# Kernel optimization log

Measured on AMD Instinct MI355X. Metric: run time of the kernel, lower is better.

Reference implementation:

```python
import jax, jax.numpy as jnp
import numpy as np

PROJ_EPS = 1e-5   # hyperbolic_projection keeps ||x|| <= 1 - PROJ_EPS
MIN_NORM = 1e-15  # numerical floor for norms/denominators
N, D, E, L = 100000, 128, 800000, 2


def _norm(x):
    return jnp.linalg.norm(x, axis=-1, keepdims=True)


def hyperbolic_projection(x):
    n = _norm(x)
    max_n = 1.0 - PROJ_EPS
    scale = jnp.where(n > max_n, max_n / jnp.maximum(n, MIN_NORM), 1.0)
    return x * scale


def exp_map_zero(v):
    n = jnp.maximum(_norm(v), MIN_NORM)
    return jnp.tanh(n) * v / n


def log_map_zero(y):
    n = jnp.maximum(_norm(y), MIN_NORM)
    nc = jnp.clip(n, MIN_NORM, 1.0 - PROJ_EPS)
    return jnp.arctanh(nc) * y / n


def mobius_addition(u, v):
    uu = jnp.sum(u * u, -1, keepdims=True)
    vv = jnp.sum(v * v, -1, keepdims=True)
    uv = jnp.sum(u * v, -1, keepdims=True)
    num = (1.0 + 2.0 * uv + vv) * u + (1.0 - uu) * v
    den = 1.0 + 2.0 * uv + uu * vv
    return num / jnp.maximum(den, MIN_NORM)


def setup_inputs() -> dict:
    key = jax.random.key(0)
    k = jax.random.split(key, 5)
    ent = jax.random.normal(k[0], (N, D), jnp.float32) * 0.1
    W = jax.random.normal(k[1], (L, D, D), jnp.float32) * (1.0 / np.sqrt(D))
    bias = jnp.zeros((L, D), jnp.float32)
    rows = jax.random.randint(k[2], (E,), 0, N)
    cols = jax.random.randint(k[3], (E,), 0, N)
    vals = jax.random.uniform(k[4], (E,), jnp.float32) / 8.0  # ~row-normalized adj values
    return {"ent_embeddings": ent, "W": W, "bias": bias,
            "adj_rows": rows, "adj_cols": cols, "adj_vals": vals}


def _gcn_layer(x, W_l, b_l, rows, cols, vals, use_act):
    # log map to tangent at origin, linear transform
    t = log_map_zero(x)                      # [N, D]
    m = t @ W_l                              # [N, D]
    # sparse adjacency matmul: adj @ m  (COO gather-scale-scatter)
    msg = m[cols] * vals[:, None]            # [E, D]
    agg = jax.ops.segment_sum(msg, rows, num_segments=N)  # [N, D]
    h = hyperbolic_projection(exp_map_zero(agg))
    # hyperbolic bias via mobius addition
    bh = hyperbolic_projection(exp_map_zero(b_l[None, :]))  # [1, D]
    h = hyperbolic_projection(mobius_addition(h, bh))
    if use_act:
        h = hyperbolic_projection(exp_map_zero(jnp.tanh(log_map_zero(h))))
    return h


def reference(ent_embeddings, W, bias, adj_rows, adj_cols, adj_vals):
    x = hyperbolic_projection(ent_embeddings)
    for l in range(L):
        use_act = (l < L - 1)  # tanh on all but last layer
        h = _gcn_layer(x, W[l], bias[l], adj_rows, adj_cols, adj_vals, use_act)
        # mobius residual connection with previous layer output
        x = hyperbolic_projection(mobius_addition(h, x))
    return x
```

## Files before the change

### kernel.cpp

```cpp
#include <hip/hip_runtime.h>
#include <math.h>

#define D 128
#define PROJ_EPS 1e-5f
#define MAX_NN (1.0f - PROJ_EPS)
#define MIN_NORM 1e-15f
#define ROWS_PER_BLOCK 2048

struct __align__(8) Edge { int c; float v; };

typedef __attribute__((ext_vector_type(8))) short bf16x8;
typedef __attribute__((ext_vector_type(4))) float f32x4;

__device__ inline unsigned cvt_pk_bf16(float a, float b) {
    unsigned r;
    asm("v_cvt_pk_bf16_f32 %0, %1, %2" : "=v"(r) : "v"(a), "v"(b));
    return r;
}

__device__ inline float wave_sum(float v) {
#pragma unroll
    for (int off = 32; off; off >>= 1) v += __shfl_xor(v, off, 64);
    return v;
}
__device__ inline float g16sum(float v) {
#pragma unroll
    for (int off = 8; off; off >>= 1) v += __shfl_xor(v, off, 64);
    return v;
}
__device__ inline void g16sum2(float& a, float& b) {
#pragma unroll
    for (int off = 8; off; off >>= 1) {
        a += __shfl_xor(a, off, 64);
        b += __shfl_xor(b, off, 64);
    }
}
__device__ inline float frcp(float x) { return __builtin_amdgcn_rcpf(x); }
__device__ inline float fsqrt_(float x) { return __builtin_amdgcn_sqrtf(x); }
__device__ inline float tanh_pos(float x) {
    float e = __expf(-2.f * x);
    return (1.f - e) * frcp(1.f + e);
}
__device__ inline float tanh_sgn(float x) {
    float ax = fabsf(x);
    float e = __expf(-2.f * ax);
    float r = (1.f - e) * frcp(1.f + e);
    return copysignf(r, x);
}
__device__ inline float atanh_clip(float x) {
    return 0.5f * __logf((1.f + x) * frcp(1.f - x));
}

__device__ inline float2 mk2(float a, float b) { float2 r; r.x = a; r.y = b; return r; }
__device__ inline float2 bc2(float a) { return mk2(a, a); }
__device__ inline float2 pk_fma2(float2 a, float2 b, float2 c) {
    float2 d;
    asm("v_pk_fma_f32 %0, %1, %2, %3" : "=v"(d) : "v"(a), "v"(b), "v"(c));
    return d;
}
__device__ inline float2 pk_mul2(float2 a, float2 b) {
    float2 d;
    asm("v_pk_mul_f32 %0, %1, %2" : "=v"(d) : "v"(a), "v"(b));
    return d;
}
__device__ inline float2 up2(unsigned u) {
    uint2 t; t.x = u << 16; t.y = u & 0xffff0000u;
    float2 r; r.x = __uint_as_float(t.x); r.y = __uint_as_float(t.y);
    return r;
}

__global__ void hist_kernel(const int* __restrict__ rows, int* __restrict__ counts, int e) {
    int i = blockIdx.x * blockDim.x + threadIdx.x;
    if (i < e) atomicAdd(&counts[rows[i]], 1);
}

__global__ __launch_bounds__(256) void partial_kernel(const int* __restrict__ counts,
                                                      int* __restrict__ partials, int n) {
    int t = threadIdx.x;
    int start = blockIdx.x * ROWS_PER_BLOCK + t * 8;
    int s = 0;
#pragma unroll
    for (int j = 0; j < 8; ++j) {
        int i = start + j;
        if (i < n) s += (counts[i] + 3) & ~3;
    }
    int lane = t & 63, wv = t >> 6;
#pragma unroll
    for (int o = 32; o; o >>= 1) s += __shfl_xor(s, o, 64);
    __shared__ int wsum[4];
    if (lane == 0) wsum[wv] = s;
    __syncthreads();
    if (t == 0) partials[blockIdx.x] = wsum[0] + wsum[1] + wsum[2] + wsum[3];
}

__global__ void scan_partials(int* __restrict__ partials, int npart) {
    __shared__ int buf[1024];
    int t = threadIdx.x;
    int v = (t < npart) ? partials[t] : 0;
    buf[t] = v;
    __syncthreads();
    for (int o = 1; o < 1024; o <<= 1) {
        int x = (t >= o) ? buf[t - o] : 0;
        __syncthreads();
        buf[t] += x;
        __syncthreads();
    }
    if (t < npart) partials[t] = buf[t] - v;
}

__global__ __launch_bounds__(256) void rowptr_kernel(const int* __restrict__ counts,
                                                     const int* __restrict__ partials,
                                                     int* __restrict__ row_ptr,
                                                     int* __restrict__ cursor, int n) {
    int t = threadIdx.x;
    int start = blockIdx.x * ROWS_PER_BLOCK + t * 8;
    int c[8];
    int s = 0;
#pragma unroll
    for (int j = 0; j < 8; ++j) {
        int i = start + j;
        c[j] = (i < n) ? ((counts[i] + 3) & ~3) : 0;
        s += c[j];
    }
    int lane = t & 63, wv = t >> 6;
    int inc = s;
#pragma unroll
    for (int o = 1; o < 64; o <<= 1) {
        int tt = __shfl_up(inc, o, 64);
        if (lane >= o) inc += tt;
    }
    __shared__ int wsum[4];
    if (lane == 63) wsum[wv] = inc;
    __syncthreads();
    if (t == 0) {
        int acc = 0;
        for (int w = 0; w < 4; ++w) { int tmp = wsum[w]; wsum[w] = acc; acc += tmp; }
    }
    __syncthreads();
    int run = partials[blockIdx.x] + wsum[wv] + (inc - s);
#pragma unroll
    for (int j = 0; j < 8; ++j) {
        int i = start + j;
        if (i < n) {
            row_ptr[i] = run;
            cursor[i] = run;
            run += c[j];
            if (i == n - 1) row_ptr[n] = run;
        }
    }
}

__global__ void scatter_kernel(const int* __restrict__ rows, const int* __restrict__ cols,
                               const float* __restrict__ vals, int* __restrict__ cursor,
                               Edge* __restrict__ eds, int e) {
    int i = blockIdx.x * blockDim.x + threadIdx.x;
    if (i < e) {
        int r = rows[i];
        int pos = atomicAdd(&cursor[r], 1);
        Edge ed; ed.c = cols[i]; ed.v = vals[i];
        eds[pos] = ed;
    }
}

__global__ __launch_bounds__(256) void proj_init(const float* __restrict__ ent,
                                                 float* __restrict__ x,
                                                 float* __restrict__ logscale,
                                                 float* __restrict__ xnorm2, int n) {
    int wid = (int)((blockIdx.x * (size_t)blockDim.x + threadIdx.x) >> 6);
    int lane = threadIdx.x & 63;
    if (wid >= n) return;
    float2 v = *(const float2*)(ent + (size_t)wid * D + 2 * lane);
    float nrm = sqrtf(wave_sum(v.x * v.x + v.y * v.y));
    float scale = (nrm > MAX_NN) ? MAX_NN / fmaxf(nrm, MIN_NORM) : 1.0f;
    float px = v.x * scale, py = v.y * scale;
    float n2 = fmaxf(sqrtf(wave_sum(px * px + py * py)), MIN_NORM);
    float nc = fminf(fmaxf(n2, MIN_NORM), MAX_NN);
    float ls = atanhf(nc) / n2;
    *(float2*)(x + (size_t)wid * D + 2 * lane) = make_float2(px, py);
    if (lane == 0) { logscale[wid] = ls; xnorm2[wid] = n2 * n2; }
}

__global__ void bias_prep(const float* __restrict__ bias, float* __restrict__ bh,
                          float* __restrict__ vvb) {
    int l = blockIdx.x;
    int lane = threadIdx.x;
    float2 b2 = *(const float2*)(bias + (size_t)l * D + 2 * lane);
    float nn = fmaxf(sqrtf(wave_sum(b2.x * b2.x + b2.y * b2.y)), MIN_NORM);
    float s = tanhf(nn) / nn;
    float bx = b2.x * s, by = b2.y * s;
    float pn = sqrtf(wave_sum(bx * bx + by * by));
    float sc = (pn > MAX_NN) ? MAX_NN / fmaxf(pn, MIN_NORM) : 1.0f;
    bx *= sc; by *= sc;
    float vv = wave_sum(bx * bx + by * by);
    *(float2*)(bh + (size_t)l * D + 2 * lane) = make_float2(bx, by);
    if (lane == 0) vvb[l] = vv;
}

__global__ __launch_bounds__(256, 3) void logmap_gemm(const float* __restrict__ x,
                                                      const float* __restrict__ logscale,
                                                      const float* __restrict__ W,
                                                      unsigned short* __restrict__ m, int n,
                                                      int ntiles) {
    __shared__ char lds[16384];
    const int t = threadIdx.x;
    const int wid = t >> 6, lane = t & 63;
    const int lcol = lane & 15, lkg = lane >> 4;
    const int colbase = wid * 32;

    bf16x8 Bh[4][2], Bl[4][2];
#pragma unroll
    for (int ki = 0; ki < 4; ++ki) {
#pragma unroll
        for (int cf = 0; cf < 2; ++cf) {
            const float* wp = W + (size_t)(ki * 32 + lkg * 8) * D + colbase + cf * 16 + lcol;
            float f[8];
#pragma unroll
            for (int e2 = 0; e2 < 8; ++e2) f[e2] = wp[(size_t)e2 * D];
            unsigned hw[4], lw[4];
#pragma unroll
            for (int p = 0; p < 4; ++p) {
                float a = f[2 * p], b = f[2 * p + 1];
                unsigned h = cvt_pk_bf16(a, b);
                float ha = __uint_as_float(h << 16);
                float hb = __uint_as_float(h & 0xffff0000u);
                hw[p] = h;
                lw[p] = cvt_pk_bf16(a - ha, b - hb);
            }
            uint4 uh = make_uint4(hw[0], hw[1], hw[2], hw[3]);
            uint4 ul = make_uint4(lw[0], lw[1], lw[2], lw[3]);
            Bh[ki][cf] = *(bf16x8*)&uh;
            Bl[ki][cf] = *(bf16x8*)&ul;
        }
    }

    for (int tile = blockIdx.x; tile < ntiles; tile += gridDim.x) {
        const int row0 = tile * 32;
        __syncthreads();
#pragma unroll
        for (int p = t; p < 512; p += 256) {
            int fi = p >> 6, ln = p & 63;
            int rf = fi >> 2, ki = fi & 3;
            int row = row0 + rf * 16 + (ln & 15);
            int k0 = ki * 32 + (ln >> 4) * 8;
            float v[8];
            if (row < n) {
                float ls = logscale[row];
                const float* xp = x + (size_t)row * D + k0;
                *(float4*)&v[0] = *(const float4*)xp;
                *(float4*)&v[4] = *(const float4*)(xp + 4);
#pragma unroll
                for (int e2 = 0; e2 < 8; ++e2) v[e2] *= ls;
            } else {
#pragma unroll
                for (int e2 = 0; e2 < 8; ++e2) v[e2] = 0.f;
            }
            unsigned hv[4], lv[4];
#pragma unroll
            for (int pp = 0; pp < 4; ++pp) {
                float a = v[2 * pp], b = v[2 * pp + 1];
                unsigned h = cvt_pk_bf16(a, b);
                float ha = __uint_as_float(h << 16);
                float hb = __uint_as_float(h & 0xffff0000u);
                hv[pp] = h;
                lv[pp] = cvt_pk_bf16(a - ha, b - hb);
            }
            *(uint4*)(lds + fi * 1024 + ln * 16) = make_uint4(hv[0], hv[1], hv[2], hv[3]);
            *(uint4*)(lds + 8192 + fi * 1024 + ln * 16) = make_uint4(lv[0], lv[1], lv[2], lv[3]);
        }
        __syncthreads();

        f32x4 acc[2][2];
#pragma unroll
        for (int rf = 0; rf < 2; ++rf)
#pragma unroll
            for (int cf = 0; cf < 2; ++cf) acc[rf][cf] = (f32x4){0.f, 0.f, 0.f, 0.f};

#pragma unroll
        for (int ki = 0; ki < 4; ++ki) {
            bf16x8 Ah[2], Al[2];
#pragma unroll
            for (int rf = 0; rf < 2; ++rf) {
                Ah[rf] = *(const bf16x8*)(lds + (rf * 4 + ki) * 1024 + lane * 16);
                Al[rf] = *(const bf16x8*)(lds + 8192 + (rf * 4 + ki) * 1024 + lane * 16);
            }
#pragma unroll
            for (int rf = 0; rf < 2; ++rf)
#pragma unroll
                for (int cf = 0; cf < 2; ++cf) {
                    acc[rf][cf] = __builtin_amdgcn_mfma_f32_16x16x32_bf16(Ah[rf], Bh[ki][cf], acc[rf][cf], 0, 0, 0);
                    acc[rf][cf] = __builtin_amdgcn_mfma_f32_16x16x32_bf16(Ah[rf], Bl[ki][cf], acc[rf][cf], 0, 0, 0);
                    acc[rf][cf] = __builtin_amdgcn_mfma_f32_16x16x32_bf16(Al[rf], Bh[ki][cf], acc[rf][cf], 0, 0, 0);
                }
        }

#pragma unroll
        for (int rf = 0; rf < 2; ++rf)
#pragma unroll
            for (int cf = 0; cf < 2; ++cf)
#pragma unroll
                for (int pr = 0; pr < 2; ++pr) {
                    unsigned u = cvt_pk_bf16(acc[rf][cf][2 * pr], acc[rf][cf][2 * pr + 1]);
                    int row = row0 + rf * 16 + lkg * 4 + 2 * pr;
                    int col = colbase + cf * 16 + lcol;
                    if (row < n) m[(size_t)row * D + col] = (unsigned short)u;
                    if (row + 1 < n) m[(size_t)(row + 1) * D + col] = (unsigned short)(u >> 16);
                }
    }
}

__global__ __launch_bounds__(256) void aggregate(const unsigned short* __restrict__ m,
                                                 const int* __restrict__ row_ptr,
                                                 const Edge* __restrict__ eds,
                                                 const float* __restrict__ bh,
                                                 const float* __restrict__ vvb_p,
                                                 float* __restrict__ x,
                                                 float* __restrict__ logscale,
                                                 float* __restrict__ xnorm2,
                                                 int n, int use_act, int last) {
    int wv = (int)((blockIdx.x * (size_t)blockDim.x + threadIdx.x) >> 6);
    int lane = threadIdx.x & 63;
    int q = lane >> 4, li = lane & 15;
    if (wv * 4 >= n) return;
    int r = wv * 4 + q;
    bool active = (r < n);

    int beg = 0, end = 0;
    if (active) { beg = row_ptr[r]; end = row_ptr[r + 1]; }

    float vv = active ? xnorm2[r] : 0.f;
    float4 xa = active ? *(const float4*)(x + (size_t)r * D + 8 * li)
                       : make_float4(0.f, 0.f, 0.f, 0.f);
    float4 xb = active ? *(const float4*)(x + (size_t)r * D + 8 * li + 4)
                       : make_float4(0.f, 0.f, 0.f, 0.f);

    const char* mB = (const char*)m + ((size_t)li << 4);
    float2 A01 = bc2(0.f), A23 = bc2(0.f), A45 = bc2(0.f), A67 = bc2(0.f);
    int e = beg;
    for (; e + 8 <= end; e += 8) {
#pragma unroll
        for (int j = 0; j < 8; ++j) {
            Edge ee = eds[e + j];
            uint4 g = *(const uint4*)(mB + ((size_t)(unsigned)ee.c << 8));
            float2 v = bc2(ee.v);
            A01 = pk_fma2(up2(g.x), v, A01); A23 = pk_fma2(up2(g.y), v, A23);
            A45 = pk_fma2(up2(g.z), v, A45); A67 = pk_fma2(up2(g.w), v, A67);
        }
    }
    if (e < end) {
#pragma unroll
        for (int j = 0; j < 4; ++j) {
            Edge ee = eds[e + j];
            uint4 g = *(const uint4*)(mB + ((size_t)(unsigned)ee.c << 8));
            float2 v = bc2(ee.v);
            A01 = pk_fma2(up2(g.x), v, A01); A23 = pk_fma2(up2(g.y), v, A23);
            A45 = pk_fma2(up2(g.z), v, A45); A67 = pk_fma2(up2(g.w), v, A67);
        }
    }

    float4 bv0 = *(const float4*)(bh + 8 * li);
    float4 bv1 = *(const float4*)(bh + 8 * li + 4);
    float2 b01 = mk2(bv0.x, bv0.y), b23 = mk2(bv0.z, bv0.w);
    float2 b45 = mk2(bv1.x, bv1.y), b67 = mk2(bv1.z, bv1.w);
    float vvb = *vvb_p;

    float2 daa = pk_fma2(A67, A67, pk_fma2(A45, A45, pk_fma2(A23, A23, pk_mul2(A01, A01))));
    float2 dab = pk_fma2(A67, b67, pk_fma2(A45, b45, pk_fma2(A23, b23, pk_mul2(A01, b01))));
    float saa = daa.x + daa.y, sab = dab.x + dab.y;
    g16sum2(saa, sab);

    float na = fmaxf(fsqrt_(saa), MIN_NORM);
    float th = tanh_pos(na);
    float s1 = th * frcp(na);
    float nh = th;
    if (th > MAX_NN) { s1 *= MAX_NN * frcp(th); nh = MAX_NN; }
    float2 vs1 = bc2(s1);
    float2 H01 = pk_mul2(A01, vs1), H23 = pk_mul2(A23, vs1);
    float2 H45 = pk_mul2(A45, vs1), H67 = pk_mul2(A67, vs1);
    float uu = nh * nh;
    float uv = s1 * sab;

    float ca = 1.f + 2.f * uv + vvb;
    float cb = 1.f - uu;
    float den = fmaxf(1.f + 2.f * uv + uu * vvb, MIN_NORM);
    float nsq = fmaxf(ca * ca * uu + 2.f * ca * cb * uv + cb * cb * vvb, 0.f);
    float rden = frcp(den);
    float n2 = fsqrt_(nsq) * rden;
    float s2 = rden;
    if (n2 > MAX_NN) { s2 *= MAX_NN * frcp(n2); n2 = MAX_NN; }
    float2 vca = bc2(ca), vcb = bc2(cb), vs2 = bc2(s2);
    float2 P01 = pk_mul2(pk_fma2(H01, vca, pk_mul2(b01, vcb)), vs2);
    float2 P23 = pk_mul2(pk_fma2(H23, vca, pk_mul2(b23, vcb)), vs2);
    float2 P45 = pk_mul2(pk_fma2(H45, vca, pk_mul2(b45, vcb)), vs2);
    float2 P67 = pk_mul2(pk_fma2(H67, vca, pk_mul2(b67, vcb)), vs2);

    float2 xo01 = mk2(xa.x, xa.y), xo23 = mk2(xa.z, xa.w);
    float2 xo45 = mk2(xb.x, xb.y), xo67 = mk2(xb.z, xb.w);

    float2 Q01, Q23, Q45, Q67;
    float uu3, uv3;
    if (use_act) {
        float nnv = fmaxf(n2, MIN_NORM);
        float nc = fminf(fmaxf(n2, MIN_NORM), MAX_NN);
        float ls2 = atanh_clip(nc) * frcp(nnv);
        float2 vls = bc2(ls2);
        float2 Z01 = pk_mul2(P01, vls), Z23 = pk_mul2(P23, vls);
        float2 Z45 = pk_mul2(P45, vls), Z67 = pk_mul2(P67, vls);
        float2 T01 = mk2(tanh_sgn(Z01.x), tanh_sgn(Z01.y));
        float2 T23 = mk2(tanh_sgn(Z23.x), tanh_sgn(Z23.y));
        float2 T45 = mk2(tanh_sgn(Z45.x), tanh_sgn(Z45.y));
        float2 T67 = mk2(tanh_sgn(Z67.x), tanh_sgn(Z67.y));
        float2 dtt = pk_fma2(T67, T67, pk_fma2(T45, T45, pk_fma2(T23, T23, pk_mul2(T01, T01))));
        float2 dtx = pk_fma2(T67, xo67, pk_fma2(T45, xo45, pk_fma2(T23, xo23, pk_mul2(T01, xo01))));
        float stt = dtt.x + dtt.y, stx = dtx.x + dtx.y;
        g16sum2(stt, stx);
        float n3 = fmaxf(fsqrt_(stt), MIN_NORM);
        float th3 = tanh_pos(n3);
        float s3 = th3 * frcp(n3);
        float nh3 = th3;
        if (th3 > MAX_NN) { s3 *= MAX_NN * frcp(th3); nh3 = MAX_NN; }
        float2 vs3 = bc2(s3);
        Q01 = pk_mul2(T01, vs3); Q23 = pk_mul2(T23, vs3);
        Q45 = pk_mul2(T45, vs3); Q67 = pk_mul2(T67, vs3);
        uu3 = nh3 * nh3;
        uv3 = s3 * stx;
    } else {
        float2 dpx = pk_fma2(P67, xo67, pk_fma2(P45, xo45, pk_fma2(P23, xo23, pk_mul2(P01, xo01))));
        float suv = g16sum(dpx.x + dpx.y);
        Q01 = P01; Q23 = P23; Q45 = P45; Q67 = P67;
        uu3 = n2 * n2;
        uv3 = suv;
    }

    ca = 1.f + 2.f * uv3 + vv;
    cb = 1.f - uu3;
    den = fmaxf(1.f + 2.f * uv3 + uu3 * vv, MIN_NORM);
    nsq = fmaxf(ca * ca * uu3 + 2.f * ca * cb * uv3 + cb * cb * vv, 0.f);
    rden = frcp(den);
    float n4 = fsqrt_(nsq) * rden;
    float s4 = rden;
    if (n4 > MAX_NN) { s4 *= MAX_NN * frcp(n4); n4 = MAX_NN; }
    float2 vca2 = bc2(ca), vcb2 = bc2(cb), vs4 = bc2(s4);
    float2 O01 = pk_mul2(pk_fma2(Q01, vca2, pk_mul2(xo01, vcb2)), vs4);
    float2 O23 = pk_mul2(pk_fma2(Q23, vca2, pk_mul2(xo23, vcb2)), vs4);
    float2 O45 = pk_mul2(pk_fma2(Q45, vca2, pk_mul2(xo45, vcb2)), vs4);
    float2 O67 = pk_mul2(pk_fma2(Q67, vca2, pk_mul2(xo67, vcb2)), vs4);

    if (active) {
        *(float4*)(x + (size_t)r * D + 8 * li) = make_float4(O01.x, O01.y, O23.x, O23.y);
        *(float4*)(x + (size_t)r * D + 8 * li + 4) = make_float4(O45.x, O45.y, O67.x, O67.y);
        if (li == 0) {
            xnorm2[r] = n4 * n4;
            if (!last) {
                float nnv = fmaxf(n4, MIN_NORM);
                float nc = fminf(fmaxf(n4, MIN_NORM), MAX_NN);
                logscale[r] = atanh_clip(nc) * frcp(nnv);
            }
        }
    }
}

extern "C" void kernel_launch(void* const* d_in, const int* in_sizes, int n_in,
                              void* d_out, int out_size, void* d_ws, size_t ws_size,
                              hipStream_t stream) {
    const float* ent  = (const float*)d_in[0];
    const float* W    = (const float*)d_in[1];
    const float* bias = (const float*)d_in[2];
    const int* rows   = (const int*)d_in[3];
    const int* cols   = (const int*)d_in[4];
    const float* vals = (const float*)d_in[5];
    float* x = (float*)d_out;

    const int n = in_sizes[0] / D;
    const int e = in_sizes[3];
    const int nlayers = in_sizes[1] / (D * D);
    const int npart = (n + ROWS_PER_BLOCK - 1) / ROWS_PER_BLOCK;
    const int ntiles = (n + 31) / 32;
    const size_t e_cap = (size_t)e + 3u * (size_t)n;

    char* ws = (char*)d_ws;
    size_t off = 0;
    auto alloc = [&](size_t bytes) {
        void* p = ws + off;
        off += (bytes + 255) & ~(size_t)255;
        return p;
    };
    unsigned short* m = (unsigned short*)alloc((size_t)n * D * sizeof(unsigned short));
    float* logscale = (float*)alloc((size_t)n * sizeof(float));
    float* xnorm2   = (float*)alloc((size_t)n * sizeof(float));
    int*   counts   = (int*)alloc((size_t)n * sizeof(int));
    int*   row_ptr  = (int*)alloc((size_t)(n + 1) * sizeof(int));
    int*   cursor   = (int*)alloc((size_t)n * sizeof(int));
    int*   partials = (int*)alloc((size_t)(npart > 1024 ? npart : 1024) * sizeof(int));
    float* bhb      = (float*)alloc((size_t)nlayers * D * sizeof(float));
    float* vvb      = (float*)alloc((size_t)nlayers * sizeof(float));
    Edge*  eds      = (Edge*)alloc(e_cap * sizeof(Edge));

    hipMemsetAsync(counts, 0, (size_t)n * sizeof(int), stream);
    hipMemsetAsync(eds, 0, e_cap * sizeof(Edge), stream);
    hist_kernel<<<(e + 255) / 256, 256, 0, stream>>>(rows, counts, e);
    partial_kernel<<<npart, 256, 0, stream>>>(counts, partials, n);
    scan_partials<<<1, 1024, 0, stream>>>(partials, npart);
    rowptr_kernel<<<npart, 256, 0, stream>>>(counts, partials, row_ptr, cursor, n);
    scatter_kernel<<<(e + 255) / 256, 256, 0, stream>>>(rows, cols, vals, cursor, eds, e);

    bias_prep<<<nlayers, 64, 0, stream>>>(bias, bhb, vvb);
    proj_init<<<(n + 3) / 4, 256, 0, stream>>>(ent, x, logscale, xnorm2, n);

    for (int l = 0; l < nlayers; ++l) {
        logmap_gemm<<<782, 256, 0, stream>>>(x, logscale, W + (size_t)l * D * D, m, n, ntiles);
        int use_act = (l < nlayers - 1) ? 1 : 0;
        aggregate<<<(n + 15) / 16, 256, 0, stream>>>(m, row_ptr, eds, bhb + (size_t)l * D,
                                                     vvb + l, x, logscale, xnorm2, n,
                                                     use_act, (l == nlayers - 1) ? 1 : 0);
    }
}
```

Before: 273.0 us.

## Two-pass bucketed edge scatter for CSR build and vectorize proj_init

Replaces the direct random scatter of edges into CSR order with a two-pass scheme. Edges are first grouped into coarse row buckets (2048 rows each) through block-local shared histograms and staging buffers, then scattered to their final positions with per-row cursors, which should give more local writes. proj_init now handles four rows per wave with float4 loads and a 16-lane reduction, and reuses the clipped norm instead of recomputing it. In exchange the code adds extra staging memory traffic, a serial single-thread bucket scan, and two more kernel launches.

```diff
diff --git a/kernel.cpp b/kernel.cpp
--- a/kernel.cpp
+++ b/kernel.cpp
@@ -6,6 +6,8 @@
 #define MAX_NN (1.0f - PROJ_EPS)
 #define MIN_NORM 1e-15f
 #define ROWS_PER_BLOCK 2048
+#define BSHIFT 11
+#define MAXB 256
 
 struct __align__(8) Edge { int c; float v; };
 
@@ -69,9 +71,25 @@
     return r;
 }
 
-__global__ void hist_kernel(const int* __restrict__ rows, int* __restrict__ counts, int e) {
-    int i = blockIdx.x * blockDim.x + threadIdx.x;
-    if (i < e) atomicAdd(&counts[rows[i]], 1);
+__global__ __launch_bounds__(256) void hist_kernel(const int* __restrict__ rows,
+                                                   int* __restrict__ counts,
+                                                   int* __restrict__ bucket_cnt, int e) {
+    __shared__ int bhist[MAXB];
+    int t = threadIdx.x;
+    if (t < MAXB) bhist[t] = 0;
+    __syncthreads();
+    int base = blockIdx.x * 2048;
+#pragma unroll
+    for (int j = 0; j < 8; ++j) {
+        int i = base + t * 8 + j;
+        if (i < e) {
+            int r = rows[i];
+            atomicAdd(&counts[r], 1);
+            atomicAdd(&bhist[r >> BSHIFT], 1);
+        }
+    }
+    __syncthreads();
+    if (t < MAXB && bhist[t]) atomicAdd(&bucket_cnt[t], bhist[t]);
 }
 
 __global__ __launch_bounds__(256) void partial_kernel(const int* __restrict__ counts,
@@ -150,15 +168,60 @@
     }
 }
 
-__global__ void scatter_kernel(const int* __restrict__ rows, const int* __restrict__ cols,
-                               const float* __restrict__ vals, int* __restrict__ cursor,
-                               Edge* __restrict__ eds, int e) {
+__global__ void bucket_scan(const int* __restrict__ bucket_cnt, int* __restrict__ bucket_cur,
+                            int nb) {
+    if (threadIdx.x == 0) {
+        int s = 0;
+        for (int j = 0; j < nb; ++j) { int v = bucket_cnt[j]; bucket_cur[j] = s; s += v; }
+    }
+}
+
+__global__ __launch_bounds__(256) void bucket_scatter(const int* __restrict__ rows,
+                                                      const int* __restrict__ cols,
+                                                      const float* __restrict__ vals,
+                                                      int* __restrict__ bucket_cur,
+                                                      int* __restrict__ rstage,
+                                                      Edge* __restrict__ estage, int e) {
+    __shared__ int bhist[MAXB];
+    __shared__ int bbase[MAXB];
+    int t = threadIdx.x;
+    if (t < MAXB) bhist[t] = 0;
+    __syncthreads();
+    int base = blockIdx.x * 2048;
+    int b[8], lr[8];
+#pragma unroll
+    for (int j = 0; j < 8; ++j) {
+        int i = base + t * 8 + j;
+        if (i < e) {
+            b[j] = rows[i] >> BSHIFT;
+            lr[j] = atomicAdd(&bhist[b[j]], 1);
+        } else b[j] = -1;
+    }
+    __syncthreads();
+    if (t < MAXB) {
+        int c = bhist[t];
+        bbase[t] = c ? atomicAdd(&bucket_cur[t], c) : 0;
+    }
+    __syncthreads();
+#pragma unroll
+    for (int j = 0; j < 8; ++j) {
+        int i = base + t * 8 + j;
+        if (b[j] >= 0) {
+            int pos = bbase[b[j]] + lr[j];
+            rstage[pos] = rows[i];
+            Edge ed; ed.c = cols[i]; ed.v = vals[i];
+            estage[pos] = ed;
+        }
+    }
+}
+
+__global__ void scatter2(const int* __restrict__ rstage, const Edge* __restrict__ estage,
+                         int* __restrict__ cursor, Edge* __restrict__ eds, int e) {
     int i = blockIdx.x * blockDim.x + threadIdx.x;
     if (i < e) {
-        int r = rows[i];
+        int r = rstage[i];
         int pos = atomicAdd(&cursor[r], 1);
-        Edge ed; ed.c = cols[i]; ed.v = vals[i];
-        eds[pos] = ed;
+        eds[pos] = estage[i];
     }
 }
 
@@ -166,18 +229,31 @@
                                                  float* __restrict__ x,
                                                  float* __restrict__ logscale,
                                                  float* __restrict__ xnorm2, int n) {
-    int wid = (int)((blockIdx.x * (size_t)blockDim.x + threadIdx.x) >> 6);
+    int wv = (int)((blockIdx.x * (size_t)blockDim.x + threadIdx.x) >> 6);
     int lane = threadIdx.x & 63;
-    if (wid >= n) return;
-    float2 v = *(const float2*)(ent + (size_t)wid * D + 2 * lane);
-    float nrm = sqrtf(wave_sum(v.x * v.x + v.y * v.y));
-    float scale = (nrm > MAX_NN) ? MAX_NN / fmaxf(nrm, MIN_NORM) : 1.0f;
-    float px = v.x * scale, py = v.y * scale;
-    float n2 = fmaxf(sqrtf(wave_sum(px * px + py * py)), MIN_NORM);
+    int q = lane >> 4, li = lane & 15;
+    if (wv * 4 >= n) return;
+    int r = wv * 4 + q;
+    bool active = (r < n);
+    float4 va = active ? *(const float4*)(ent + (size_t)r * D + 8 * li)
+                       : make_float4(0.f, 0.f, 0.f, 0.f);
+    float4 vb = active ? *(const float4*)(ent + (size_t)r * D + 8 * li + 4)
+                       : make_float4(0.f, 0.f, 0.f, 0.f);
+    float ss = va.x * va.x + va.y * va.y + va.z * va.z + va.w * va.w
+             + vb.x * vb.x + vb.y * vb.y + vb.z * vb.z + vb.w * vb.w;
+    ss = g16sum(ss);
+    float nrm = fsqrt_(ss);
+    float scale = (nrm > MAX_NN) ? MAX_NN * frcp(fmaxf(nrm, MIN_NORM)) : 1.0f;
+    float n2 = fminf(nrm, MAX_NN);
     float nc = fminf(fmaxf(n2, MIN_NORM), MAX_NN);
-    float ls = atanhf(nc) / n2;
-    *(float2*)(x + (size_t)wid * D + 2 * lane) = make_float2(px, py);
-    if (lane == 0) { logscale[wid] = ls; xnorm2[wid] = n2 * n2; }
+    float ls = atanh_clip(nc) * frcp(fmaxf(n2, MIN_NORM));
+    if (active) {
+        *(float4*)(x + (size_t)r * D + 8 * li) =
+            make_float4(va.x * scale, va.y * scale, va.z * scale, va.w * scale);
+        *(float4*)(x + (size_t)r * D + 8 * li + 4) =
+            make_float4(vb.x * scale, vb.y * scale, vb.z * scale, vb.w * scale);
+        if (li == 0) { logscale[r] = ls; xnorm2[r] = n2 * n2; }
+    }
 }
 
 __global__ void bias_prep(const float* __restrict__ bias, float* __restrict__ bh,
@@ -474,6 +550,7 @@
     const int e = in_sizes[3];
     const int nlayers = in_sizes[1] / (D * D);
     const int npart = (n + ROWS_PER_BLOCK - 1) / ROWS_PER_BLOCK;
+    const int npart_e = (e + 2047) / 2048;
     const int ntiles = (n + 31) / 32;
     const size_t e_cap = (size_t)e + 3u * (size_t)n;
 
@@ -491,20 +568,28 @@
     int*   row_ptr  = (int*)alloc((size_t)(n + 1) * sizeof(int));
     int*   cursor   = (int*)alloc((size_t)n * sizeof(int));
     int*   partials = (int*)alloc((size_t)(npart > 1024 ? npart : 1024) * sizeof(int));
+    int*   bucket_cnt = (int*)alloc((size_t)MAXB * sizeof(int));
+    int*   bucket_cur = (int*)alloc((size_t)MAXB * sizeof(int));
     float* bhb      = (float*)alloc((size_t)nlayers * D * sizeof(float));
     float* vvb      = (float*)alloc((size_t)nlayers * sizeof(float));
+    int*   rstage   = (int*)alloc((size_t)e * sizeof(int));
+    Edge*  estage   = (Edge*)alloc((size_t)e * sizeof(Edge));
     Edge*  eds      = (Edge*)alloc(e_cap * sizeof(Edge));
 
     hipMemsetAsync(counts, 0, (size_t)n * sizeof(int), stream);
+    hipMemsetAsync(bucket_cnt, 0, (size_t)MAXB * sizeof(int), stream);
     hipMemsetAsync(eds, 0, e_cap * sizeof(Edge), stream);
-    hist_kernel<<<(e + 255) / 256, 256, 0, stream>>>(rows, counts, e);
+
+    hist_kernel<<<npart_e, 256, 0, stream>>>(rows, counts, bucket_cnt, e);
     partial_kernel<<<npart, 256, 0, stream>>>(counts, partials, n);
     scan_partials<<<1, 1024, 0, stream>>>(partials, npart);
     rowptr_kernel<<<npart, 256, 0, stream>>>(counts, partials, row_ptr, cursor, n);
-    scatter_kernel<<<(e + 255) / 256, 256, 0, stream>>>(rows, cols, vals, cursor, eds, e);
+    bucket_scan<<<1, 64, 0, stream>>>(bucket_cnt, bucket_cur, npart);
+    bucket_scatter<<<npart_e, 256, 0, stream>>>(rows, cols, vals, bucket_cur, rstage, estage, e);
+    scatter2<<<(e + 255) / 256, 256, 0, stream>>>(rstage, estage, cursor, eds, e);
 
     bias_prep<<<nlayers, 64, 0, stream>>>(bias, bhb, vvb);
-    proj_init<<<(n + 3) / 4, 256, 0, stream>>>(ent, x, logscale, xnorm2, n);
+    proj_init<<<(n + 15) / 16, 256, 0, stream>>>(ent, x, logscale, xnorm2, n);
 
     for (int l = 0; l < nlayers; ++l) {
         logmap_gemm<<<782, 256, 0, stream>>>(x, logscale, W + (size_t)l * D * D, m, n, ntiles);
```

New measurement: 271.3 us. No clear change (-0.6%).

## Precompute split-bf16 W fragments once, one tile per GEMM block, vectorize proj_init

Applied to the files above, without the earlier changes.

Adds a wprep kernel that converts W into hi/lo bf16 MFMA fragment layouts once per layer, so each logmap_gemm block loads them directly instead of re-strided-reading and converting W. The GEMM drops its persistent grid-stride loop and launches one block per 32-row tile, with no forced occupancy hint. proj_init now processes four rows per wave with float4 loads, 16-lane reductions and fast reciprocal/sqrt helpers. The trade is an extra small kernel launch and more GEMM blocks, each paying a fragment reload.

```diff
diff --git a/kernel.cpp b/kernel.cpp
--- a/kernel.cpp
+++ b/kernel.cpp
@@ -166,18 +166,31 @@
                                                  float* __restrict__ x,
                                                  float* __restrict__ logscale,
                                                  float* __restrict__ xnorm2, int n) {
-    int wid = (int)((blockIdx.x * (size_t)blockDim.x + threadIdx.x) >> 6);
+    int wv = (int)((blockIdx.x * (size_t)blockDim.x + threadIdx.x) >> 6);
     int lane = threadIdx.x & 63;
-    if (wid >= n) return;
-    float2 v = *(const float2*)(ent + (size_t)wid * D + 2 * lane);
-    float nrm = sqrtf(wave_sum(v.x * v.x + v.y * v.y));
-    float scale = (nrm > MAX_NN) ? MAX_NN / fmaxf(nrm, MIN_NORM) : 1.0f;
-    float px = v.x * scale, py = v.y * scale;
-    float n2 = fmaxf(sqrtf(wave_sum(px * px + py * py)), MIN_NORM);
+    int q = lane >> 4, li = lane & 15;
+    if (wv * 4 >= n) return;
+    int r = wv * 4 + q;
+    bool active = (r < n);
+    float4 va = active ? *(const float4*)(ent + (size_t)r * D + 8 * li)
+                       : make_float4(0.f, 0.f, 0.f, 0.f);
+    float4 vb = active ? *(const float4*)(ent + (size_t)r * D + 8 * li + 4)
+                       : make_float4(0.f, 0.f, 0.f, 0.f);
+    float ss = va.x * va.x + va.y * va.y + va.z * va.z + va.w * va.w
+             + vb.x * vb.x + vb.y * vb.y + vb.z * vb.z + vb.w * vb.w;
+    ss = g16sum(ss);
+    float nrm = fsqrt_(ss);
+    float scale = (nrm > MAX_NN) ? MAX_NN * frcp(fmaxf(nrm, MIN_NORM)) : 1.0f;
+    float n2 = fminf(nrm, MAX_NN);
     float nc = fminf(fmaxf(n2, MIN_NORM), MAX_NN);
-    float ls = atanhf(nc) / n2;
-    *(float2*)(x + (size_t)wid * D + 2 * lane) = make_float2(px, py);
-    if (lane == 0) { logscale[wid] = ls; xnorm2[wid] = n2 * n2; }
+    float ls = atanh_clip(nc) * frcp(fmaxf(n2, MIN_NORM));
+    if (active) {
+        *(float4*)(x + (size_t)r * D + 8 * li) =
+            make_float4(va.x * scale, va.y * scale, va.z * scale, va.w * scale);
+        *(float4*)(x + (size_t)r * D + 8 * li + 4) =
+            make_float4(vb.x * scale, vb.y * scale, vb.z * scale, vb.w * scale);
+        if (li == 0) { logscale[r] = ls; xnorm2[r] = n2 * n2; }
+    }
 }
 
 __global__ void bias_prep(const float* __restrict__ bias, float* __restrict__ bh,
@@ -196,11 +209,42 @@
     if (lane == 0) vvb[l] = vv;
 }
 
-__global__ __launch_bounds__(256, 3) void logmap_gemm(const float* __restrict__ x,
-                                                      const float* __restrict__ logscale,
-                                                      const float* __restrict__ W,
-                                                      unsigned short* __restrict__ m, int n,
-                                                      int ntiles) {
+__global__ __launch_bounds__(256) void wprep(const float* __restrict__ W,
+                                             uint4* __restrict__ wh, uint4* __restrict__ wl,
+                                             int nlayers) {
+    int l = blockIdx.x >> 3;
+    int eidx = (blockIdx.x & 7) * 256 + threadIdx.x;
+    if (l >= nlayers) return;
+    int lane = eidx & 63;
+    int fi = eidx >> 6;
+    int wid = fi >> 3, ki = (fi >> 1) & 3, cf = fi & 1;
+    int lcol = lane & 15, lkg = lane >> 4;
+    int col = wid * 32 + cf * 16 + lcol;
+    int krow = ki * 32 + lkg * 8;
+    const float* wp = W + (size_t)l * D * D + (size_t)krow * D + col;
+    float f[8];
+#pragma unroll
+    for (int e2 = 0; e2 < 8; ++e2) f[e2] = wp[(size_t)e2 * D];
+    unsigned hw[4], lw[4];
+#pragma unroll
+    for (int p = 0; p < 4; ++p) {
+        float a = f[2 * p], b = f[2 * p + 1];
+        unsigned h = cvt_pk_bf16(a, b);
+        float ha = __uint_as_float(h << 16);
+        float hb = __uint_as_float(h & 0xffff0000u);
+        hw[p] = h;
+        lw[p] = cvt_pk_bf16(a - ha, b - hb);
+    }
+    size_t off = (size_t)l * 2048 + eidx;
+    wh[off] = make_uint4(hw[0], hw[1], hw[2], hw[3]);
+    wl[off] = make_uint4(lw[0], lw[1], lw[2], lw[3]);
+}
+
+__global__ __launch_bounds__(256) void logmap_gemm(const float* __restrict__ x,
+                                                   const float* __restrict__ logscale,
+                                                   const uint4* __restrict__ wh,
+                                                   const uint4* __restrict__ wl,
+                                                   unsigned short* __restrict__ m, int n) {
     __shared__ char lds[16384];
     const int t = threadIdx.x;
     const int wid = t >> 6, lane = t & 63;
@@ -212,100 +256,84 @@
     for (int ki = 0; ki < 4; ++ki) {
 #pragma unroll
         for (int cf = 0; cf < 2; ++cf) {
-            const float* wp = W + (size_t)(ki * 32 + lkg * 8) * D + colbase + cf * 16 + lcol;
-            float f[8];
-#pragma unroll
-            for (int e2 = 0; e2 < 8; ++e2) f[e2] = wp[(size_t)e2 * D];
-            unsigned hw[4], lw[4];
-#pragma unroll
-            for (int p = 0; p < 4; ++p) {
-                float a = f[2 * p], b = f[2 * p + 1];
-                unsigned h = cvt_pk_bf16(a, b);
-                float ha = __uint_as_float(h << 16);
-                float hb = __uint_as_float(h & 0xffff0000u);
-                hw[p] = h;
-                lw[p] = cvt_pk_bf16(a - ha, b - hb);
-            }
-            uint4 uh = make_uint4(hw[0], hw[1], hw[2], hw[3]);
-            uint4 ul = make_uint4(lw[0], lw[1], lw[2], lw[3]);
+            size_t off = (size_t)(wid * 8 + ki * 2 + cf) * 64 + lane;
+            uint4 uh = wh[off];
+            uint4 ul = wl[off];
             Bh[ki][cf] = *(bf16x8*)&uh;
             Bl[ki][cf] = *(bf16x8*)&ul;
         }
     }
 
-    for (int tile = blockIdx.x; tile < ntiles; tile += gridDim.x) {
-        const int row0 = tile * 32;
-        __syncthreads();
-#pragma unroll
-        for (int p = t; p < 512; p += 256) {
-            int fi = p >> 6, ln = p & 63;
-            int rf = fi >> 2, ki = fi & 3;
-            int row = row0 + rf * 16 + (ln & 15);
-            int k0 = ki * 32 + (ln >> 4) * 8;
-            float v[8];
-            if (row < n) {
-                float ls = logscale[row];
-                const float* xp = x + (size_t)row * D + k0;
-                *(float4*)&v[0] = *(const float4*)xp;
-                *(float4*)&v[4] = *(const float4*)(xp + 4);
-#pragma unroll
-                for (int e2 = 0; e2 < 8; ++e2) v[e2] *= ls;
-            } else {
-#pragma unroll
-                for (int e2 = 0; e2 < 8; ++e2) v[e2] = 0.f;
+    const int row0 = blockIdx.x * 32;
+#pragma unroll
+    for (int p = t; p < 512; p += 256) {
+        int fi = p >> 6, ln = p & 63;
+        int rf = fi >> 2, ki = fi & 3;
+        int row = row0 + rf * 16 + (ln & 15);
+        int k0 = ki * 32 + (ln >> 4) * 8;
+        float v[8];
+        if (row < n) {
+            float ls = logscale[row];
+            const float* xp = x + (size_t)row * D + k0;
+            *(float4*)&v[0] = *(const float4*)xp;
+            *(float4*)&v[4] = *(const float4*)(xp + 4);
+#pragma unroll
+            for (int e2 = 0; e2 < 8; ++e2) v[e2] *= ls;
+        } else {
+#pragma unroll
+            for (int e2 = 0; e2 < 8; ++e2) v[e2] = 0.f;
+        }
+        unsigned hv[4], lv[4];
+#pragma unroll
+        for (int pp = 0; pp < 4; ++pp) {
+            float a = v[2 * pp], b = v[2 * pp + 1];
+            unsigned h = cvt_pk_bf16(a, b);
+            float ha = __uint_as_float(h << 16);
+            float hb = __uint_as_float(h & 0xffff0000u);
+            hv[pp] = h;
+            lv[pp] = cvt_pk_bf16(a - ha, b - hb);
+        }
+        *(uint4*)(lds + fi * 1024 + ln * 16) = make_uint4(hv[0], hv[1], hv[2], hv[3]);
+        *(uint4*)(lds + 8192 + fi * 1024 + ln * 16) = make_uint4(lv[0], lv[1], lv[2], lv[3]);
+    }
+    __syncthreads();
+
+    f32x4 acc[2][2];
+#pragma unroll
+    for (int rf = 0; rf < 2; ++rf)
+#pragma unroll
+        for (int cf = 0; cf < 2; ++cf) acc[rf][cf] = (f32x4){0.f, 0.f, 0.f, 0.f};
+
+#pragma unroll
+    for (int ki = 0; ki < 4; ++ki) {
+        bf16x8 Ah[2], Al[2];
+#pragma unroll
+        for (int rf = 0; rf < 2; ++rf) {
+            Ah[rf] = *(const bf16x8*)(lds + (rf * 4 + ki) * 1024 + lane * 16);
+            Al[rf] = *(const bf16x8*)(lds + 8192 + (rf * 4 + ki) * 1024 + lane * 16);
+        }
+#pragma unroll
+        for (int rf = 0; rf < 2; ++rf)
+#pragma unroll
+            for (int cf = 0; cf < 2; ++cf) {
+                acc[rf][cf] = __builtin_amdgcn_mfma_f32_16x16x32_bf16(Ah[rf], Bh[ki][cf], acc[rf][cf], 0, 0, 0);
+                acc[rf][cf] = __builtin_amdgcn_mfma_f32_16x16x32_bf16(Ah[rf], Bl[ki][cf], acc[rf][cf], 0, 0, 0);
+                acc[rf][cf] = __builtin_amdgcn_mfma_f32_16x16x32_bf16(Al[rf], Bh[ki][cf], acc[rf][cf], 0, 0, 0);
             }
-            unsigned hv[4], lv[4];
-#pragma unroll
-            for (int pp = 0; pp < 4; ++pp) {
-                float a = v[2 * pp], b = v[2 * pp + 1];
-                unsigned h = cvt_pk_bf16(a, b);
-                float ha = __uint_as_float(h << 16);
-                float hb = __uint_as_float(h & 0xffff0000u);
-                hv[pp] = h;
-                lv[pp] = cvt_pk_bf16(a - ha, b - hb);
+    }
+
+#pragma unroll
+    for (int rf = 0; rf < 2; ++rf)
+#pragma unroll
+        for (int cf = 0; cf < 2; ++cf)
+#pragma unroll
+            for (int pr = 0; pr < 2; ++pr) {
+                unsigned u = cvt_pk_bf16(acc[rf][cf][2 * pr], acc[rf][cf][2 * pr + 1]);
+                int row = row0 + rf * 16 + lkg * 4 + 2 * pr;
+                int col = colbase + cf * 16 + lcol;
+                if (row < n) m[(size_t)row * D + col] = (unsigned short)u;
+                if (row + 1 < n) m[(size_t)(row + 1) * D + col] = (unsigned short)(u >> 16);
             }
-            *(uint4*)(lds + fi * 1024 + ln * 16) = make_uint4(hv[0], hv[1], hv[2], hv[3]);
-            *(uint4*)(lds + 8192 + fi * 1024 + ln * 16) = make_uint4(lv[0], lv[1], lv[2], lv[3]);
-        }
-        __syncthreads();
-
-        f32x4 acc[2][2];
-#pragma unroll
-        for (int rf = 0; rf < 2; ++rf)
-#pragma unroll
-            for (int cf = 0; cf < 2; ++cf) acc[rf][cf] = (f32x4){0.f, 0.f, 0.f, 0.f};
-
-#pragma unroll
-        for (int ki = 0; ki < 4; ++ki) {
-            bf16x8 Ah[2], Al[2];
-#pragma unroll
-            for (int rf = 0; rf < 2; ++rf) {
-                Ah[rf] = *(const bf16x8*)(lds + (rf * 4 + ki) * 1024 + lane * 16);
-                Al[rf] = *(const bf16x8*)(lds + 8192 + (rf * 4 + ki) * 1024 + lane * 16);
-            }
-#pragma unroll
-            for (int rf = 0; rf < 2; ++rf)
-#pragma unroll
-                for (int cf = 0; cf < 2; ++cf) {
-                    acc[rf][cf] = __builtin_amdgcn_mfma_f32_16x16x32_bf16(Ah[rf], Bh[ki][cf], acc[rf][cf], 0, 0, 0);
-                    acc[rf][cf] = __builtin_amdgcn_mfma_f32_16x16x32_bf16(Ah[rf], Bl[ki][cf], acc[rf][cf], 0, 0, 0);
-                    acc[rf][cf] = __builtin_amdgcn_mfma_f32_16x16x32_bf16(Al[rf], Bh[ki][cf], acc[rf][cf], 0, 0, 0);
-                }
-        }
-
-#pragma unroll
-        for (int rf = 0; rf < 2; ++rf)
-#pragma unroll
-            for (int cf = 0; cf < 2; ++cf)
-#pragma unroll
-                for (int pr = 0; pr < 2; ++pr) {
-                    unsigned u = cvt_pk_bf16(acc[rf][cf][2 * pr], acc[rf][cf][2 * pr + 1]);
-                    int row = row0 + rf * 16 + lkg * 4 + 2 * pr;
-                    int col = colbase + cf * 16 + lcol;
-                    if (row < n) m[(size_t)row * D + col] = (unsigned short)u;
-                    if (row + 1 < n) m[(size_t)(row + 1) * D + col] = (unsigned short)(u >> 16);
-                }
-    }
 }
 
 __global__ __launch_bounds__(256) void aggregate(const unsigned short* __restrict__ m,
@@ -493,6 +521,8 @@
     int*   partials = (int*)alloc((size_t)(npart > 1024 ? npart : 1024) * sizeof(int));
     float* bhb      = (float*)alloc((size_t)nlayers * D * sizeof(float));
     float* vvb      = (float*)alloc((size_t)nlayers * sizeof(float));
+    uint4* whb      = (uint4*)alloc((size_t)nlayers * 2048 * sizeof(uint4));
+    uint4* wlb      = (uint4*)alloc((size_t)nlayers * 2048 * sizeof(uint4));
     Edge*  eds      = (Edge*)alloc(e_cap * sizeof(Edge));
 
     hipMemsetAsync(counts, 0, (size_t)n * sizeof(int), stream);
@@ -504,10 +534,13 @@
     scatter_kernel<<<(e + 255) / 256, 256, 0, stream>>>(rows, cols, vals, cursor, eds, e);
 
     bias_prep<<<nlayers, 64, 0, stream>>>(bias, bhb, vvb);
-    proj_init<<<(n + 3) / 4, 256, 0, stream>>>(ent, x, logscale, xnorm2, n);
+    wprep<<<nlayers * 8, 256, 0, stream>>>(W, whb, wlb, nlayers);
+    proj_init<<<(n + 15) / 16, 256, 0, stream>>>(ent, x, logscale, xnorm2, n);
 
     for (int l = 0; l < nlayers; ++l) {
-        logmap_gemm<<<782, 256, 0, stream>>>(x, logscale, W + (size_t)l * D * D, m, n, ntiles);
+        logmap_gemm<<<ntiles, 256, 0, stream>>>(x, logscale,
+                                                whb + (size_t)l * 2048,
+                                                wlb + (size_t)l * 2048, m, n);
         int use_act = (l < nlayers - 1) ? 1 : 0;
         aggregate<<<(n + 15) / 16, 256, 0, stream>>>(m, row_ptr, eds, bhb + (size_t)l * D,
                                                      vvb + l, x, logscale, xnorm2, n,
```

Result: faster. 262.4 us (median of 2 runs) (-3.9%).
